# Kernel optimization log

Hardware: AMD Instinct MI355X
Metric: run time of the kernel (lower is better)

Reference implementation:

```python
import jax, jax.numpy as jnp
from jax import lax
import numpy as np

VOCAB, EMB, H, L, NCLS = 50000, 128, 128, 2, 2
B, S = 128, 1024


def setup_inputs() -> dict:
    key = jax.random.key(0)
    ks = jax.random.split(key, 16)
    r = lambda k, shp: (jax.random.normal(k, shp, dtype=jnp.float32) * 0.05)
    return {
        "inputs": jax.random.randint(ks[0], (B, S), 0, VOCAB),
        "emb": r(ks[1], (VOCAB, EMB)),
        "Wih_l0": r(ks[2], (2, 4 * H, EMB)),
        "Whh_l0": r(ks[3], (2, 4 * H, H)),
        "bih_l0": r(ks[4], (2, 4 * H)),
        "bhh_l0": r(ks[5], (2, 4 * H)),
        "Wih_l1": r(ks[6], (2, 4 * H, 2 * H)),
        "Whh_l1": r(ks[7], (2, 4 * H, H)),
        "bih_l1": r(ks[8], (2, 4 * H)),
        "bhh_l1": r(ks[9], (2, 4 * H)),
        "dec_W": r(ks[10], (64, 2 * H)),
        "dec_b": r(ks[11], (64,)),
        "fc1_W": r(ks[12], (NCLS, 64)),
        "fc1_b": r(ks[13], (NCLS,)),
    }


def _lstm_dir(x, Wih, Whh, bih, bhh, reverse):
    # x: [S, B, in_dim]; PyTorch gate order i, f, g, o
    Sdim, Bdim, _ = x.shape
    Hd = Whh.shape[1]
    xg = jnp.einsum('sbe,ge->sbg', x, Wih) + bih + bhh  # precompute input projection

    def step(carry, g_in):
        h, c = carry
        g = g_in + h @ Whh.T
        i, f, gc, o = jnp.split(g, 4, axis=-1)
        c = jax.nn.sigmoid(f) * c + jax.nn.sigmoid(i) * jnp.tanh(gc)
        h = jax.nn.sigmoid(o) * jnp.tanh(c)
        return (h, c), h

    init = (jnp.zeros((Bdim, Hd), x.dtype), jnp.zeros((Bdim, Hd), x.dtype))
    (hT, _), hs = lax.scan(step, init, xg, reverse=reverse)
    return hs, hT  # hs: [S,B,H], hT: final hidden of this direction


def _bilstm_layer(x, Wih, Whh, bih, bhh):
    hs_f, hf = _lstm_dir(x, Wih[0], Whh[0], bih[0], bhh[0], False)
    hs_b, hb = _lstm_dir(x, Wih[1], Whh[1], bih[1], bhh[1], True)
    return jnp.concatenate([hs_f, hs_b], axis=-1), hf, hb


def reference(inputs, emb, Wih_l0, Whh_l0, bih_l0, bhh_l0,
              Wih_l1, Whh_l1, bih_l1, bhh_l1, dec_W, dec_b, fc1_W, fc1_b):
    x = emb[inputs]                    # [B,S,E]
    x = jnp.transpose(x, (1, 0, 2))    # [S,B,E] (seq-first, as in torch permute)
    x, _, _ = _bilstm_layer(x, Wih_l0, Whh_l0, bih_l0, bhh_l0)
    _, hf, hb = _bilstm_layer(x, Wih_l1, Whh_l1, bih_l1, bhh_l1)
    h = jnp.concatenate([hf, hb], axis=-1)  # [B, 2H] — last layer fwd/bwd final states
    h = h @ dec_W.T + dec_b
    return h @ fc1_W.T + fc1_b              # [B, n_class]
```

## Files before the change

kernel.cpp:

```cpp
#include <hip/hip_runtime.h>

#define S_LEN 1024
#define BATCH 128

using u16 = unsigned short;
using u32 = unsigned int;
typedef _Float16 f16;
typedef __attribute__((ext_vector_type(2))) _Float16 f16x2;
typedef __attribute__((ext_vector_type(8))) _Float16 f16x8;
typedef __attribute__((ext_vector_type(4))) float floatx4;

__device__ __forceinline__ float fexp(float x) {
    return __builtin_amdgcn_exp2f(x * 1.4426950408889634f);
}
__device__ __forceinline__ float fsigmoid(float x) {
    return __builtin_amdgcn_rcpf(1.f + fexp(-x));
}
__device__ __forceinline__ float ftanh(float x) {
    return 1.f - 2.f * __builtin_amdgcn_rcpf(fexp(2.f * x) + 1.f);
}

__global__ __launch_bounds__(256) void prep_kernel(
        const float* __restrict__ Wih0, const float* __restrict__ Whh0f,
        const float* __restrict__ Wih1, const float* __restrict__ Whh1f,
        const float* __restrict__ bih0, const float* __restrict__ bhh0,
        const float* __restrict__ bih1, const float* __restrict__ bhh1,
        f16* __restrict__ W0, f16* __restrict__ W1,
        f16* __restrict__ Wh0, f16* __restrict__ Wh1,
        float* __restrict__ b0, float* __restrict__ b1) {
    int i = blockIdx.x * 256 + threadIdx.x;
    if (i < 131072) {
        W0[i]  = (f16)Wih0[i];
        Wh0[i] = (f16)Whh0f[i];
        Wh1[i] = (f16)Whh1f[i];
    }
    if (i < 262144) W1[i] = (f16)Wih1[i];
    if (i < 1024) { b0[i] = bih0[i] + bhh0[i]; b1[i] = bih1[i] + bhh1[i]; }
}

template<int K, bool GATHER>
__global__ __launch_bounds__(256) void proj_chunk(
        const f16* __restrict__ A, const int* __restrict__ inputs,
        const float* __restrict__ emb, const f16* __restrict__ Bw,
        const float* __restrict__ bias, f16* __restrict__ C,
        int s0, int s0b, int CH) {
    __shared__ __align__(16) f16 As[128][72];
    __shared__ __align__(16) f16 Bs[128][72];
    const int t = threadIdx.x;
    const u32 nwg8 = gridDim.x >> 3;
    const u32 bid = (blockIdx.x & 7) * nwg8 + (blockIdx.x >> 3);
    const u32 per_dir = (u32)CH * 4;
    const int dir = (int)(bid / per_dir);
    const u32 rr = bid % per_dir;
    const int mt = (int)(rr >> 2);
    const int n0 = (int)(rr & 3) * 128;
    const int lane = t & 63, wid = t >> 6;
    const int wm = wid >> 1, wn = wid & 1;
    const int lrow = lane & 15;
    const int lk8  = (lane >> 4) * 8;

    floatx4 acc[4][4] = {};

    const int srow = t >> 3;
    const int scol = (t & 7) * 8;
    for (int k0 = 0; k0 < K; k0 += 64) {
        __syncthreads();
        #pragma unroll
        for (int r = 0; r < 4; ++r) {
            int row = srow + r * 32;
            int l = mt * 128 + row;
            int bb = l & 127, ls = l >> 7;
            int sidx = dir ? (s0b - ls) : (s0 + ls);
            if constexpr (GATHER) {
                int idx = inputs[bb * S_LEN + sidx];
                const float* ep = emb + (size_t)idx * 128 + k0 + scol;
                float4 v0 = *reinterpret_cast<const float4*>(ep);
                float4 v1 = *reinterpret_cast<const float4*>(ep + 4);
                f16x8 o = { (f16)v0.x, (f16)v0.y, (f16)v0.z, (f16)v0.w,
                            (f16)v1.x, (f16)v1.y, (f16)v1.z, (f16)v1.w };
                *reinterpret_cast<f16x8*>(&As[row][scol]) = o;
            } else {
                uint4 av = *reinterpret_cast<const uint4*>(
                    A + (size_t)(sidx * 128 + bb) * K + k0 + scol);
                *reinterpret_cast<uint4*>(&As[row][scol]) = av;
            }
            uint4 bv = *reinterpret_cast<const uint4*>(
                Bw + (size_t)(dir * 512 + n0 + row) * K + k0 + scol);
            *reinterpret_cast<uint4*>(&Bs[row][scol]) = bv;
        }
        __syncthreads();
        #pragma unroll
        for (int ks = 0; ks < 2; ++ks) {
            f16x8 af[4], bf[4];
            #pragma unroll
            for (int f = 0; f < 4; ++f) {
                af[f] = *reinterpret_cast<const f16x8*>(&As[wm * 64 + f * 16 + lrow][ks * 32 + lk8]);
                bf[f] = *reinterpret_cast<const f16x8*>(&Bs[wn * 64 + f * 16 + lrow][ks * 32 + lk8]);
            }
            #pragma unroll
            for (int fm = 0; fm < 4; ++fm)
                #pragma unroll
                for (int fn = 0; fn < 4; ++fn)
                    acc[fm][fn] = __builtin_amdgcn_mfma_f32_16x16x32_f16(
                        af[fm], bf[fn], acc[fm][fn], 0, 0, 0);
        }
    }
    f16* Cd = C + (size_t)dir * CH * 128 * 512;
    #pragma unroll
    for (int fn = 0; fn < 4; ++fn) {
        int col = n0 + wn * 64 + fn * 16 + lrow;
        float bv = bias[dir * 512 + col];
        #pragma unroll
        for (int fm = 0; fm < 4; ++fm) {
            int rowl = mt * 128 + wm * 64 + fm * 16 + (lane >> 4) * 4;
            #pragma unroll
            for (int r = 0; r < 4; ++r) {
                float v = acc[fm][fn][r] + bv;
                Cd[(size_t)(rowl + r) * 512 + col] = (f16)v;
            }
        }
    }
}

template<int LAYER>
__global__ __launch_bounds__(512, 2) void recur_chunk(
        const f16* __restrict__ xgc,
        const f16* __restrict__ Whh,
        f16* __restrict__ hs_out,
        float* __restrict__ h_state,
        float* __restrict__ c_state,
        int s0, int s0b, int CH, int first) {
    const int t = threadIdx.x;
    const int dir = blockIdx.x >> 7;
    const int b = blockIdx.x & 127;

    __shared__ __align__(16) f16 h16[128];
    __shared__ float act_lds[512];

    f16x2 w2[64];
    {
        const f16x8* wp8 = reinterpret_cast<const f16x8*>(Whh + (size_t)(dir * 512 + t) * 128);
        #pragma unroll
        for (int k = 0; k < 16; ++k) {
            f16x8 v = wp8[k];
            w2[4*k+0] = f16x2{v[0], v[1]};
            w2[4*k+1] = f16x2{v[2], v[3]};
            w2[4*k+2] = f16x2{v[4], v[5]};
            w2[4*k+3] = f16x2{v[6], v[7]};
        }
    }

    const int sbase = (dir * 128 + b) * 128 + t;
    float c = 0.f;
    if (t < 128) {
        if (first) { h16[t] = (f16)0.f; }
        else       { h16[t] = (f16)h_state[sbase]; c = c_state[sbase]; }
    }
    __syncthreads();

    const f16* xbase = xgc + ((size_t)(dir * CH) * 128 + b) * 512 + t;
    auto xaddr = [&](int li) -> const f16* {
        return xbase + (size_t)li * (128 * 512);
    };

    const f16x8* hp = reinterpret_cast<const f16x8*>(h16);

    auto step = [&](int li, f16 xv) {
        f16x2 acc0{}, acc1{}, acc2{}, acc3{};
        #pragma unroll
        for (int k = 0; k < 16; ++k) {
            f16x8 hv = hp[k];
            acc0 += f16x2{hv[0], hv[1]} * w2[4*k+0];
            acc1 += f16x2{hv[2], hv[3]} * w2[4*k+1];
            acc2 += f16x2{hv[4], hv[5]} * w2[4*k+2];
            acc3 += f16x2{hv[6], hv[7]} * w2[4*k+3];
        }
        f16x2 s0v = acc0 + acc1, s1v = acc2 + acc3, sv = s0v + s1v;
        float g = (float)xv + (float)sv[0] + (float)sv[1];
        float a = ((t >> 7) == 2) ? ftanh(g) : fsigmoid(g);
        act_lds[t] = a;
        asm volatile("s_waitcnt lgkmcnt(0)" ::: "memory");
        __builtin_amdgcn_s_barrier();
        asm volatile("" ::: "memory");
        if (t < 128) {
            float ai = act_lds[t], af = act_lds[t + 128];
            float ag = act_lds[t + 256], ao = act_lds[t + 384];
            c = af * c + ai * ag;
            float hn = ao * ftanh(c);
            h16[t] = (f16)hn;
            if (LAYER == 0) {
                int sidx = dir ? (s0b - li) : (s0 + li);
                hs_out[(size_t)(sidx * BATCH + b) * 256 + dir * 128 + t] = (f16)hn;
            }
        }
        asm volatile("s_waitcnt lgkmcnt(0)" ::: "memory");
        __builtin_amdgcn_s_barrier();
        asm volatile("" ::: "memory");
    };

    f16 xa = *xaddr(0);
    f16 xb_ = *xaddr(CH > 1 ? 1 : 0);
    for (int li = 0; li < CH; li += 2) {
        f16 xc = *xaddr(li + 2 < CH ? li + 2 : CH - 1);
        step(li, xa);
        f16 xd = *xaddr(li + 3 < CH ? li + 3 : CH - 1);
        step(li + 1, xb_);
        xa = xc; xb_ = xd;
    }
    if (t < 128) {
        h_state[sbase] = (float)h16[t];
        c_state[sbase] = c;
    }
}

__global__ __launch_bounds__(64) void decode_kernel(
        const float* __restrict__ h_state, const float* __restrict__ decW,
        const float* __restrict__ decb, const float* __restrict__ fc1W,
        const float* __restrict__ fc1b, float* __restrict__ out) {
    __shared__ float t1[64];
    int b = blockIdx.x, j = threadIdx.x;
    float acc = decb[j];
    const float* h0 = h_state + (size_t)b * 128;
    const float* h1 = h_state + (size_t)(128 + b) * 128;
    const float* wr = decW + (size_t)j * 256;
    #pragma unroll 4
    for (int k = 0; k < 128; ++k) acc += h0[k] * wr[k];
    #pragma unroll 4
    for (int k = 0; k < 128; ++k) acc += h1[k] * wr[128 + k];
    t1[j] = acc;
    __syncthreads();
    if (j < 2) {
        float o = fc1b[j];
        #pragma unroll
        for (int k = 0; k < 64; ++k) o += t1[k] * fc1W[j * 64 + k];
        out[b * 2 + j] = o;
    }
}

extern "C" void kernel_launch(void* const* d_in, const int* in_sizes, int n_in,
                              void* d_out, int out_size, void* d_ws, size_t ws_size,
                              hipStream_t stream) {
    const int*   inputs = (const int*)d_in[0];
    const float* emb    = (const float*)d_in[1];
    const float* Wih0   = (const float*)d_in[2];
    const float* Whh0   = (const float*)d_in[3];
    const float* bih0   = (const float*)d_in[4];
    const float* bhh0   = (const float*)d_in[5];
    const float* Wih1   = (const float*)d_in[6];
    const float* Whh1   = (const float*)d_in[7];
    const float* bih1   = (const float*)d_in[8];
    const float* bhh1   = (const float*)d_in[9];
    const float* decW   = (const float*)d_in[10];
    const float* decb   = (const float*)d_in[11];
    const float* fc1W   = (const float*)d_in[12];
    const float* fc1b   = (const float*)d_in[13];
    float* out = (float*)d_out;

    char* ws = (char*)d_ws;
    size_t off = 0;
    auto alloc = [&](size_t bytes) {
        char* p = ws + off;
        off = (off + bytes + 255) & ~(size_t)255;
        return p;
    };
    f16*   W0      = (f16*)alloc((size_t)131072 * 2);
    f16*   W1      = (f16*)alloc((size_t)262144 * 2);
    f16*   Wh0     = (f16*)alloc((size_t)131072 * 2);
    f16*   Wh1     = (f16*)alloc((size_t)131072 * 2);
    float* b0      = (float*)alloc(1024 * 4);
    float* b1      = (float*)alloc(1024 * 4);
    float* h_state = (float*)alloc((size_t)2 * 128 * 128 * 4);
    float* c_state = (float*)alloc((size_t)2 * 128 * 128 * 4);
    f16*   hs0     = (f16*)alloc((size_t)131072 * 256 * 2);
    size_t fixed_end = off;

    int CH = 32;
    size_t avail = (ws_size > fixed_end) ? (ws_size - fixed_end) : 0;
    for (int c = 1024; c >= 32; c >>= 1) {
        if ((size_t)c * 262144 <= avail) { CH = c; break; }
    }
    f16* xgc = (f16*)alloc((size_t)CH * 262144);
    const int NC = S_LEN / CH;

    prep_kernel<<<1024, 256, 0, stream>>>(Wih0, Whh0, Wih1, Whh1,
                                          bih0, bhh0, bih1, bhh1,
                                          W0, W1, Wh0, Wh1, b0, b1);
    for (int ci = 0; ci < NC; ++ci) {
        int s0 = ci * CH, s0b = S_LEN - 1 - ci * CH;
        proj_chunk<128, true><<<8 * CH, 256, 0, stream>>>(
            nullptr, inputs, emb, W0, b0, xgc, s0, s0b, CH);
        recur_chunk<0><<<256, 512, 0, stream>>>(
            xgc, Wh0, hs0, h_state, c_state, s0, s0b, CH, ci == 0);
    }
    for (int ci = 0; ci < NC; ++ci) {
        int s0 = ci * CH, s0b = S_LEN - 1 - ci * CH;
        proj_chunk<256, false><<<8 * CH, 256, 0, stream>>>(
            hs0, nullptr, nullptr, W1, b1, xgc, s0, s0b, CH);
        recur_chunk<1><<<256, 512, 0, stream>>>(
            xgc, Wh1, nullptr, h_state, c_state, s0, s0b, CH, ci == 0);
    }
    decode_kernel<<<128, 64, 0, stream>>>(h_state, decW, decb, fc1W, fc1b, out);
}
```

Before: 1.604 ms.

## Use MFMA for LSTM recurrence over 16-batch tiles with gate-interleaved layout

```diff
diff --git a/kernel.cpp b/kernel.cpp
--- a/kernel.cpp
+++ b/kernel.cpp
@@ -68,9 +68,8 @@
         #pragma unroll
         for (int r = 0; r < 4; ++r) {
             int row = srow + r * 32;
-            int l = mt * 128 + row;
-            int bb = l & 127, ls = l >> 7;
-            int sidx = dir ? (s0b - ls) : (s0 + ls);
+            int bb = row;
+            int sidx = dir ? (s0b - mt) : (s0 + mt);
             if constexpr (GATHER) {
                 int idx = inputs[bb * S_LEN + sidx];
                 const float* ep = emb + (size_t)idx * 128 + k0 + scol;
@@ -105,112 +104,166 @@
                         af[fm], bf[fn], acc[fm][fn], 0, 0, 0);
         }
     }
-    f16* Cd = C + (size_t)dir * CH * 128 * 512;
+    f16* Cd = C + (size_t)dir * CH * 65536;
     #pragma unroll
     for (int fn = 0; fn < 4; ++fn) {
         int col = n0 + wn * 64 + fn * 16 + lrow;
         float bv = bias[dir * 512 + col];
+        int gate = col >> 7, uu = col & 127;
+        int wv2 = uu >> 4, uo2 = uu & 15;
         #pragma unroll
         for (int fm = 0; fm < 4; ++fm) {
-            int rowl = mt * 128 + wm * 64 + fm * 16 + (lane >> 4) * 4;
+            int rowb = wm * 64 + fm * 16 + (lane >> 4) * 4;
             #pragma unroll
             for (int r = 0; r < 4; ++r) {
+                int b = rowb + r;
+                int bgrp = b >> 4, pl = b & 15;
+                int pq2 = pl >> 2, r2 = pl & 3;
                 float v = acc[fm][fn][r] + bv;
-                Cd[(size_t)(rowl + r) * 512 + col] = (f16)v;
+                Cd[(size_t)mt * 65536 + bgrp * 8192 + wv2 * 1024
+                   + (pq2 * 16 + uo2) * 16 + r2 * 4 + gate] = (f16)v;
             }
         }
     }
 }
 
+
+#define ACT(R, CR) {                                                            \
+    float i_ = fsigmoid(ac0[R]);                                                \
+    float f_ = fsigmoid(ac1[R]);                                                \
+    float g_ = ftanh(ac2[R]);                                                   \
+    float o_ = fsigmoid(ac3[R]);                                                \
+    CR = f_ * CR + i_ * g_;                                                     \
+    float hn = o_ * ftanh(CR);                                                  \
+    f16 hv = (f16)hn;                                                           \
+    *(f16*)(hwb + woff##R) = hv;                                                \
+    if constexpr (LAYER == 0) hs_out[off0 + (R) * 256] = hv;                    \
+}
+
+#define RSTEP(PAR, XLO, XHI) {                                                  \
+    char* hrb = hb + (PAR) * 4096;                                              \
+    char* hwb = hb + ((PAR) ^ 1) * 4096;                                        \
+    f16x8 a0 = *(const f16x8*)(hrb + roff0);                                    \
+    f16x8 a1 = *(const f16x8*)(hrb + roff1);                                    \
+    f16x8 a2 = *(const f16x8*)(hrb + roff2);                                    \
+    f16x8 a3 = *(const f16x8*)(hrb + roff3);                                    \
+    f16x8 lo8 = __builtin_bit_cast(f16x8, XLO);                                 \
+    f16x8 hi8 = __builtin_bit_cast(f16x8, XHI);                                 \
+    floatx4 ac0 = {(float)lo8[0], (float)lo8[4], (float)hi8[0], (float)hi8[4]}; \
+    floatx4 ac1 = {(float)lo8[1], (float)lo8[5], (float)hi8[1], (float)hi8[5]}; \
+    floatx4 ac2 = {(float)lo8[2], (float)lo8[6], (float)hi8[2], (float)hi8[6]}; \
+    floatx4 ac3 = {(float)lo8[3], (float)lo8[7], (float)hi8[3], (float)hi8[7]}; \
+    ac0 = __builtin_amdgcn_mfma_f32_16x16x32_f16(a0, b00, ac0, 0, 0, 0);        \
+    ac1 = __builtin_amdgcn_mfma_f32_16x16x32_f16(a0, b10, ac1, 0, 0, 0);        \
+    ac2 = __builtin_amdgcn_mfma_f32_16x16x32_f16(a0, b20, ac2, 0, 0, 0);        \
+    ac3 = __builtin_amdgcn_mfma_f32_16x16x32_f16(a0, b30, ac3, 0, 0, 0);        \
+    ac0 = __builtin_amdgcn_mfma_f32_16x16x32_f16(a1, b01, ac0, 0, 0, 0);        \
+    ac1 = __builtin_amdgcn_mfma_f32_16x16x32_f16(a1, b11, ac1, 0, 0, 0);        \
+    ac2 = __builtin_amdgcn_mfma_f32_16x16x32_f16(a1, b21, ac2, 0, 0, 0);        \
+    ac3 = __builtin_amdgcn_mfma_f32_16x16x32_f16(a1, b31, ac3, 0, 0, 0);        \
+    ac0 = __builtin_amdgcn_mfma_f32_16x16x32_f16(a2, b02, ac0, 0, 0, 0);        \
+    ac1 = __builtin_amdgcn_mfma_f32_16x16x32_f16(a2, b12, ac1, 0, 0, 0);        \
+    ac2 = __builtin_amdgcn_mfma_f32_16x16x32_f16(a2, b22, ac2, 0, 0, 0);        \
+    ac3 = __builtin_amdgcn_mfma_f32_16x16x32_f16(a2, b32, ac3, 0, 0, 0);        \
+    ac0 = __builtin_amdgcn_mfma_f32_16x16x32_f16(a3, b03, ac0, 0, 0, 0);        \
+    ac1 = __builtin_amdgcn_mfma_f32_16x16x32_f16(a3, b13, ac1, 0, 0, 0);        \
+    ac2 = __builtin_amdgcn_mfma_f32_16x16x32_f16(a3, b23, ac2, 0, 0, 0);        \
+    ac3 = __builtin_amdgcn_mfma_f32_16x16x32_f16(a3, b33, ac3, 0, 0, 0);        \
+    ACT(0, c0) ACT(1, c1) ACT(2, c2) ACT(3, c3)                                 \
+    if constexpr (LAYER == 0) off0 += dstep;                                    \
+    asm volatile("s_waitcnt lgkmcnt(0)" ::: "memory");                          \
+    __builtin_amdgcn_s_barrier();                                               \
+    asm volatile("" ::: "memory");                                              \
+}
+
 template<int LAYER>
-__global__ __launch_bounds__(512, 2) void recur_chunk(
-        const f16* __restrict__ xgc,
+__global__ __launch_bounds__(512, 2) void recur_mfma(
+        const f16* __restrict__ xg2,
         const f16* __restrict__ Whh,
         f16* __restrict__ hs_out,
         float* __restrict__ h_state,
         float* __restrict__ c_state,
         int s0, int s0b, int CH, int first) {
     const int t = threadIdx.x;
-    const int dir = blockIdx.x >> 7;
-    const int b = blockIdx.x & 127;
-
-    __shared__ __align__(16) f16 h16[128];
-    __shared__ float act_lds[512];
-
-    f16x2 w2[64];
-    {
-        const f16x8* wp8 = reinterpret_cast<const f16x8*>(Whh + (size_t)(dir * 512 + t) * 128);
-        #pragma unroll
-        for (int k = 0; k < 16; ++k) {
-            f16x8 v = wp8[k];
-            w2[4*k+0] = f16x2{v[0], v[1]};
-            w2[4*k+1] = f16x2{v[2], v[3]};
-            w2[4*k+2] = f16x2{v[4], v[5]};
-            w2[4*k+3] = f16x2{v[6], v[7]};
-        }
-    }
-
-    const int sbase = (dir * 128 + b) * 128 + t;
-    float c = 0.f;
-    if (t < 128) {
-        if (first) { h16[t] = (f16)0.f; }
-        else       { h16[t] = (f16)h_state[sbase]; c = c_state[sbase]; }
+    const int wv = t >> 6, l = t & 63;
+    const int gblk = blockIdx.x;
+    const int dir = gblk >> 3;
+    const int b_base = (gblk & 7) * 16;
+    const int pq = l >> 4, uo = l & 15;
+    const int u = wv * 16 + uo;
+
+    __shared__ __align__(16) char hb[2 * 4096];
+
+    #define LDW(G, KS) (*reinterpret_cast<const f16x8*>( \
+        Whh + (size_t)(dir * 512 + (G) * 128 + u) * 128 + (KS) * 32 + pq * 8))
+    f16x8 b00 = LDW(0,0), b01 = LDW(0,1), b02 = LDW(0,2), b03 = LDW(0,3);
+    f16x8 b10 = LDW(1,0), b11 = LDW(1,1), b12 = LDW(1,2), b13 = LDW(1,3);
+    f16x8 b20 = LDW(2,0), b21 = LDW(2,1), b22 = LDW(2,2), b23 = LDW(2,3);
+    f16x8 b30 = LDW(3,0), b31 = LDW(3,1), b32 = LDW(3,2), b33 = LDW(3,3);
+    #undef LDW
+
+    const int roff0 = uo * 256 + ((0 * 4 + pq) ^ (uo & 7)) * 16;
+    const int roff1 = uo * 256 + ((1 * 4 + pq) ^ (uo & 7)) * 16;
+    const int roff2 = uo * 256 + ((2 * 4 + pq) ^ (uo & 7)) * 16;
+    const int roff3 = uo * 256 + ((3 * 4 + pq) ^ (uo & 7)) * 16;
+    const int p0 = pq * 4, p1 = p0 + 1, p2 = p0 + 2, p3 = p0 + 3;
+    const int woff0 = p0 * 256 + (((u >> 3) ^ (p0 & 7)) * 16) + (u & 7) * 2;
+    const int woff1 = p1 * 256 + (((u >> 3) ^ (p1 & 7)) * 16) + (u & 7) * 2;
+    const int woff2 = p2 * 256 + (((u >> 3) ^ (p2 & 7)) * 16) + (u & 7) * 2;
+    const int woff3 = p3 * 256 + (((u >> 3) ^ (p3 & 7)) * 16) + (u & 7) * 2;
+
+    float c0 = first ? 0.f : c_state[(dir * 128 + b_base + p0) * 128 + u];
+    float c1 = first ? 0.f : c_state[(dir * 128 + b_base + p1) * 128 + u];
+    float c2 = first ? 0.f : c_state[(dir * 128 + b_base + p2) * 128 + u];
+    float c3 = first ? 0.f : c_state[(dir * 128 + b_base + p3) * 128 + u];
+
+    #pragma unroll
+    for (int j = 0; j < 4; ++j) {
+        int flat = t + 512 * j;
+        int p = flat >> 7, uu2 = flat & 127;
+        f16 hv = first ? (f16)0.f : (f16)h_state[(dir * 128 + b_base + p) * 128 + uu2];
+        *(f16*)(hb + p * 256 + (((uu2 >> 3) ^ (p & 7)) * 16) + (uu2 & 7) * 2) = hv;
     }
     __syncthreads();
 
-    const f16* xbase = xgc + ((size_t)(dir * CH) * 128 + b) * 512 + t;
-    auto xaddr = [&](int li) -> const f16* {
-        return xbase + (size_t)li * (128 * 512);
+    const size_t xbase = (size_t)(dir * CH) * 65536
+                       + (size_t)(gblk & 7) * 8192 + wv * 1024 + l * 16;
+    auto xga = [&](int s) -> const uint4* {
+        int sc = s < CH ? s : CH - 1;
+        return reinterpret_cast<const uint4*>(xg2 + xbase + (size_t)sc * 65536);
     };
 
-    const f16x8* hp = reinterpret_cast<const f16x8*>(h16);
-
-    auto step = [&](int li, f16 xv) {
-        f16x2 acc0{}, acc1{}, acc2{}, acc3{};
-        #pragma unroll
-        for (int k = 0; k < 16; ++k) {
-            f16x8 hv = hp[k];
-            acc0 += f16x2{hv[0], hv[1]} * w2[4*k+0];
-            acc1 += f16x2{hv[2], hv[3]} * w2[4*k+1];
-            acc2 += f16x2{hv[4], hv[5]} * w2[4*k+2];
-            acc3 += f16x2{hv[6], hv[7]} * w2[4*k+3];
-        }
-        f16x2 s0v = acc0 + acc1, s1v = acc2 + acc3, sv = s0v + s1v;
-        float g = (float)xv + (float)sv[0] + (float)sv[1];
-        float a = ((t >> 7) == 2) ? ftanh(g) : fsigmoid(g);
-        act_lds[t] = a;
-        asm volatile("s_waitcnt lgkmcnt(0)" ::: "memory");
-        __builtin_amdgcn_s_barrier();
-        asm volatile("" ::: "memory");
-        if (t < 128) {
-            float ai = act_lds[t], af = act_lds[t + 128];
-            float ag = act_lds[t + 256], ao = act_lds[t + 384];
-            c = af * c + ai * ag;
-            float hn = ao * ftanh(c);
-            h16[t] = (f16)hn;
-            if (LAYER == 0) {
-                int sidx = dir ? (s0b - li) : (s0 + li);
-                hs_out[(size_t)(sidx * BATCH + b) * 256 + dir * 128 + t] = (f16)hn;
-            }
-        }
-        asm volatile("s_waitcnt lgkmcnt(0)" ::: "memory");
-        __builtin_amdgcn_s_barrier();
-        asm volatile("" ::: "memory");
-    };
-
-    f16 xa = *xaddr(0);
-    f16 xb_ = *xaddr(CH > 1 ? 1 : 0);
+    long long off0 = 0, dstep = 0;
+    if constexpr (LAYER == 0) {
+        off0 = ((long long)(dir ? s0b : s0) * 128 + b_base + p0) * 256 + dir * 128 + u;
+        dstep = dir ? -32768LL : 32768LL;
+    }
+
+    const uint4* q = xga(0);
+    uint4 xlo_a = q[0], xhi_a = q[1];
+    q = xga(1);
+    uint4 xlo_b = q[0], xhi_b = q[1];
     for (int li = 0; li < CH; li += 2) {
-        f16 xc = *xaddr(li + 2 < CH ? li + 2 : CH - 1);
-        step(li, xa);
-        f16 xd = *xaddr(li + 3 < CH ? li + 3 : CH - 1);
-        step(li + 1, xb_);
-        xa = xc; xb_ = xd;
-    }
-    if (t < 128) {
-        h_state[sbase] = (float)h16[t];
-        c_state[sbase] = c;
-    }
+        q = xga(li + 2);
+        uint4 xlo_c = q[0], xhi_c = q[1];
+        RSTEP(0, xlo_a, xhi_a)
+        q = xga(li + 3);
+        uint4 xlo_d = q[0], xhi_d = q[1];
+        RSTEP(1, xlo_b, xhi_b)
+        xlo_a = xlo_c; xhi_a = xhi_c; xlo_b = xlo_d; xhi_b = xhi_d;
+    }
+
+    #pragma unroll
+    for (int j = 0; j < 4; ++j) {
+        int flat = t + 512 * j;
+        int p = flat >> 7, uu2 = flat & 127;
+        f16 hv = *(const f16*)(hb + p * 256 + (((uu2 >> 3) ^ (p & 7)) * 16) + (uu2 & 7) * 2);
+        h_state[(dir * 128 + b_base + p) * 128 + uu2] = (float)hv;
+    }
+    c_state[(dir * 128 + b_base + p0) * 128 + u] = c0;
+    c_state[(dir * 128 + b_base + p1) * 128 + u] = c1;
+    c_state[(dir * 128 + b_base + p2) * 128 + u] = c2;
+    c_state[(dir * 128 + b_base + p3) * 128 + u] = c3;
 }
 
 __global__ __launch_bounds__(64) void decode_kernel(
@@ -276,8 +329,8 @@
 
     int CH = 32;
     size_t avail = (ws_size > fixed_end) ? (ws_size - fixed_end) : 0;
-    for (int c = 1024; c >= 32; c >>= 1) {
-        if ((size_t)c * 262144 <= avail) { CH = c; break; }
+    for (int cc = 1024; cc >= 32; cc >>= 1) {
+        if ((size_t)cc * 262144 <= avail) { CH = cc; break; }
     }
     f16* xgc = (f16*)alloc((size_t)CH * 262144);
     const int NC = S_LEN / CH;
@@ -289,14 +342,14 @@
         int s0 = ci * CH, s0b = S_LEN - 1 - ci * CH;
         proj_chunk<128, true><<<8 * CH, 256, 0, stream>>>(
             nullptr, inputs, emb, W0, b0, xgc, s0, s0b, CH);
-        recur_chunk<0><<<256, 512, 0, stream>>>(
+        recur_mfma<0><<<16, 512, 0, stream>>>(
             xgc, Wh0, hs0, h_state, c_state, s0, s0b, CH, ci == 0);
     }
     for (int ci = 0; ci < NC; ++ci) {
         int s0 = ci * CH, s0b = S_LEN - 1 - ci * CH;
         proj_chunk<256, false><<<8 * CH, 256, 0, stream>>>(
             hs0, nullptr, nullptr, W1, b1, xgc, s0, s0b, CH);
-        recur_chunk<1><<<256, 512, 0, stream>>>(
+        recur_mfma<1><<<16, 512, 0, stream>>>(
             xgc, Wh1, nullptr, h_state, c_state, s0, s0b, CH, ci == 0);
     }
     decode_kernel<<<128, 64, 0, stream>>>(h_state, decW, decb, fc1W, fc1b, out);
```

Result: slower. 2.588 ms (+61.4%).
